# Kernel optimization log

Measured on AMD Instinct MI355X. Metric: run time of the kernel, lower is better.

Reference implementation:

```python
import jax, jax.numpy as jnp
import numpy as np

NUM_GROUPS = 32
EPS = 1e-6


def setup_inputs() -> dict:
    key = jax.random.key(0)
    ks = jax.random.split(key, 10)
    B, C, L = 8, 512, 4096
    s = 1.0 / np.sqrt(C)
    x = jax.random.normal(ks[0], (B, C, L), dtype=jnp.float32)
    gn_w = jnp.ones((C,), jnp.float32)
    gn_b = jnp.zeros((C,), jnp.float32)
    wq = jax.random.normal(ks[1], (C, C), jnp.float32) * s
    bq = jax.random.normal(ks[2], (C,), jnp.float32) * 0.01
    wk = jax.random.normal(ks[3], (C, C), jnp.float32) * s
    bk = jax.random.normal(ks[4], (C,), jnp.float32) * 0.01
    wv = jax.random.normal(ks[5], (C, C), jnp.float32) * s
    bv = jax.random.normal(ks[6], (C,), jnp.float32) * 0.01
    wo = jax.random.normal(ks[7], (C, C), jnp.float32) * s
    bo = jax.random.normal(ks[8], (C,), jnp.float32) * 0.01
    return {"x": x, "gn_w": gn_w, "gn_b": gn_b, "wq": wq, "bq": bq,
            "wk": wk, "bk": bk, "wv": wv, "bv": bv, "wo": wo, "bo": bo}


def _group_norm(x, w, b):
    # x: [B, C, L]; normalize over each group's (C/G, L) slice
    B, C, L = x.shape
    g = x.reshape(B, NUM_GROUPS, C // NUM_GROUPS, L)
    mu = jnp.mean(g, axis=(2, 3), keepdims=True)
    var = jnp.var(g, axis=(2, 3), keepdims=True)
    g = (g - mu) * jax.lax.rsqrt(var + EPS)
    return g.reshape(B, C, L) * w[None, :, None] + b[None, :, None]


def _conv1x1(h, w, b):
    # pointwise conv: [B,C,L] x [Cout,Cin] -> [B,Cout,L]
    return jnp.einsum('oc,bcl->bol', w, h) + b[None, :, None]


def reference(x, gn_w, gn_b, wq, bq, wk, bk, wv, bv, wo, bo):
    h = _group_norm(x, gn_w, gn_b)
    q = _conv1x1(h, wq, bq)
    k = _conv1x1(h, wk, bk)
    v = _conv1x1(h, wv, bv)
    B, C, L = q.shape
    scale = jnp.asarray(C, q.dtype) ** -0.5
    # w_[b,i,j] = sum_c q[b,c,i] k[b,c,j]
    w_ = jnp.einsum('bci,bcj->bij', q, k) * scale
    w_ = jax.nn.softmax(w_, axis=2)
    # h[b,c,i] = sum_j v[b,c,j] w_[b,i,j]
    h = jnp.einsum('bcj,bij->bci', v, w_)
    return x + _conv1x1(h, wo, bo)
```

## Files before the change

kernel.cpp:

```cpp
#include <hip/hip_runtime.h>
#include <hip/hip_bf16.h>
#include <math.h>

#define DI __device__ __forceinline__

typedef unsigned short u16;
typedef unsigned int   u32;
typedef unsigned long long u64;
typedef __attribute__((ext_vector_type(8))) short short8;
typedef __attribute__((ext_vector_type(4))) float f32x4;

constexpr int CB = 512;
constexpr int LL = 4096;
constexpr int NG = 32;

DI float bf2f(u16 u) { u32 v = ((u32)u) << 16; float f; __builtin_memcpy(&f, &v, 4); return f; }
DI u16 f2bf(float f) {
  u32 u; __builtin_memcpy(&u, &f, 4);
  u += 0x7fffu + ((u >> 16) & 1u);
  return (u16)(u >> 16);
}

DI void gload16(const void* g, void* l) {
  __builtin_amdgcn_global_load_lds((const __attribute__((address_space(1))) u32*)g,
                                   (__attribute__((address_space(3))) u32*)l, 16, 0, 0);
}

__global__ __launch_bounds__(256) void conv_w(
    const float* __restrict__ wq, const float* __restrict__ wk,
    const float* __restrict__ wv, const float* __restrict__ wo,
    const float* __restrict__ bq, const float* __restrict__ bk,
    const float* __restrict__ bv,
    u16* __restrict__ wqkv, u16* __restrict__ wob, float* __restrict__ bqkv) {
  if (blockIdx.x < 1024) {
    int i = blockIdx.x * 256 + threadIdx.x;
    wqkv[i]          = f2bf(wq[i]);
    wqkv[262144 + i] = f2bf(wk[i]);
    wqkv[524288 + i] = f2bf(wv[i]);
    wob[i]           = f2bf(wo[i]);
  } else {
    for (int j = 0; j < 6; ++j) {
      int idx = j * 256 + threadIdx.x;
      float b = (idx < 512) ? bq[idx] : (idx < 1024) ? bk[idx - 512] : bv[idx - 1024];
      bqkv[idx] = b;
    }
  }
}

__global__ __launch_bounds__(256) void gn_stats(const float* __restrict__ x,
                                                float* __restrict__ stats) {
  const float4* base = (const float4*)(x + (long)blockIdx.x * (16 * LL));
  float s = 0.f, ss = 0.f;
  for (int i = threadIdx.x; i < 16 * LL / 4; i += 256) {
    float4 v = base[i];
    s  += v.x + v.y + v.z + v.w;
    ss += v.x * v.x + v.y * v.y + v.z * v.z + v.w * v.w;
  }
#pragma unroll
  for (int o = 32; o; o >>= 1) { s += __shfl_xor(s, o); ss += __shfl_xor(ss, o); }
  __shared__ float red[8];
  int wv = threadIdx.x >> 6, ln = threadIdx.x & 63;
  if (ln == 0) { red[wv * 2] = s; red[wv * 2 + 1] = ss; }
  __syncthreads();
  if (threadIdx.x == 0) {
    float S = red[0] + red[2] + red[4] + red[6];
    float SS = red[1] + red[3] + red[5] + red[7];
    float mu = S * (1.f / 65536.f);
    float var = SS * (1.f / 65536.f) - mu * mu;
    stats[blockIdx.x * 2]     = mu;
    stats[blockIdx.x * 2 + 1] = rsqrtf(var + 1e-6f);
  }
}

__global__ __launch_bounds__(256) void gn_apply(
    const float* __restrict__ x, const float* __restrict__ gw,
    const float* __restrict__ gb, const float* __restrict__ stats,
    u16* __restrict__ hT) {
  __shared__ u16 t[64][66];
  const int b = blockIdx.z, c0 = blockIdx.y * 64, l0 = blockIdx.x * 64;
  const int ln = threadIdx.x & 63, sub = threadIdx.x >> 6;
  for (int cr = sub; cr < 64; cr += 4) {
    int c = c0 + cr;
    float v  = x[(long)b * CB * LL + (long)c * LL + l0 + ln];
    float mu = stats[(b * NG + (c >> 4)) * 2];
    float rs = stats[(b * NG + (c >> 4)) * 2 + 1];
    t[cr][ln] = f2bf((v - mu) * rs * gw[c] + gb[c]);
  }
  __syncthreads();
  for (int lr = sub; lr < 64; lr += 4)
    hT[(long)b * LL * CB + (long)(l0 + lr) * CB + c0 + ln] = t[ln][lr];
}

template <int Q>
DI void rdA(const u16* LB, int wr, int fr, int fq, short8 af[2][2]) {
#pragma unroll
  for (int m2 = 0; m2 < 2; ++m2)
#pragma unroll
    for (int kk = 0; kk < 2; ++kk) {
      const int R = wr * 128 + (Q * 2 + m2) * 16 + fr;
      af[m2][kk] = *(const short8*)((const char*)LB + R * 128 +
                                    ((kk * 64 + fq * 16) ^ ((R & 7) << 4)));
    }
}
DI void rdB(const u16* LB, int wc, int fr, int fq, short8 bf[4][2]) {
#pragma unroll
  for (int nf = 0; nf < 4; ++nf)
#pragma unroll
    for (int kk = 0; kk < 2; ++kk) {
      const int R = wc * 64 + nf * 16 + fr;
      bf[nf][kk] = *(const short8*)((const char*)LB + R * 128 +
                                    ((kk * 64 + fq * 16) ^ ((R & 7) << 4)));
    }
}
template <int Q>
DI void mmaQ(short8 af[2][2], short8 bf[4][2], f32x4 acc[8][4]) {
#pragma unroll
  for (int kk = 0; kk < 2; ++kk)
#pragma unroll
    for (int m2 = 0; m2 < 2; ++m2)
#pragma unroll
      for (int nf = 0; nf < 4; ++nf)
        acc[Q * 2 + m2][nf] = __builtin_amdgcn_mfma_f32_16x16x32_bf16(
            af[m2][kk], bf[nf][kk], acc[Q * 2 + m2][nf], 0, 0, 0);
}

#define PTAIL(Q)                                             \
  __builtin_amdgcn_s_barrier();                              \
  asm volatile("s_waitcnt lgkmcnt(0)" ::: "memory");         \
  __builtin_amdgcn_sched_barrier(0);                         \
  __builtin_amdgcn_s_setprio(1);                             \
  mmaQ<Q>(af, bf, acc);                                      \
  __builtin_amdgcn_s_setprio(0);                             \
  __builtin_amdgcn_s_barrier();

template <int EPI>
__global__ __launch_bounds__(512, 2) void gemm8p(
    const u16* __restrict__ A, int lda, long asb,
    const u16* __restrict__ Bt, int ldb, long bsb,
    int K, const float* __restrict__ bias, float scale,
    u16* __restrict__ o0, u16* __restrict__ o1, u16* __restrict__ o2,
    long osb, int ldo) {
  __shared__ u16 smem[65536];
  u16* lA0 = smem;
  u16* lA1 = smem + 16384;
  u16* lB0 = smem + 32768;
  u16* lB1 = smem + 49152;

  const int tid = threadIdx.x;
  const int lane = tid & 63, wv = tid >> 6;
  const int wr = wv >> 2, wc = wv & 3;
  const int fr = lane & 15, fq = lane >> 4;
  const int bx = blockIdx.x, by = blockIdx.y, bz = blockIdx.z;

  const u16* Ab = A + (long)bz * asb + (long)(by * 256) * lda;
  const u16* Bb = Bt + (long)bz * bsb + (long)(bx * 256) * ldb;

  auto stage = [&](u16* lbase, const u16* gbase, int ld_, int half, int t) {
#pragma unroll
    for (int p = 0; p < 2; ++p) {
      int i = p * 512 + tid;
      int row = i >> 3, ch = i & 7;
      int src = t * 64 + ((((ch << 4) ^ ((row & 7) << 4))) >> 1);
      gload16(gbase + (long)(half * 128 + row) * ld_ + src,
              lbase + half * 8192 + i * 8);
    }
  };

  f32x4 acc[8][4];
#pragma unroll
  for (int m = 0; m < 8; ++m)
#pragma unroll
    for (int n = 0; n < 4; ++n) acc[m][n] = (f32x4)(0.f);

  stage(lA0, Ab, lda, 0, 0); stage(lA0, Ab, lda, 1, 0);
  stage(lB0, Bb, ldb, 0, 0); stage(lB0, Bb, ldb, 1, 0);
  stage(lB1, Bb, ldb, 0, 1); stage(lB1, Bb, ldb, 1, 1);
  asm volatile("s_waitcnt vmcnt(4)" ::: "memory");
  __builtin_amdgcn_sched_barrier(0);
  __builtin_amdgcn_s_barrier();

  const int nt = K >> 6;
  short8 af[2][2], bf[4][2];
  for (int i = 0; i < nt / 2; ++i) {
    const bool last = (i == nt / 2 - 1);
    const int t1 = 2 * i + 1, t2 = 2 * i + 2, t3 = 2 * i + 3;
    rdB(lB0, wc, fr, fq, bf);
    rdA<0>(lA0, wr, fr, fq, af);
    stage(lA1, Ab, lda, 0, t1);
    PTAIL(0)
    rdA<1>(lA0, wr, fr, fq, af);
    stage(lA1, Ab, lda, 1, t1);
    PTAIL(1)
    rdA<2>(lA0, wr, fr, fq, af);
    if (!last) stage(lB0, Bb, ldb, 0, t2);
    PTAIL(2)
    rdA<3>(lA0, wr, fr, fq, af);
    if (!last) stage(lB0, Bb, ldb, 1, t2);
    if (last) { asm volatile("s_waitcnt vmcnt(0)" ::: "memory"); }
    else      { asm volatile("s_waitcnt vmcnt(4)" ::: "memory"); }
    __builtin_amdgcn_sched_barrier(0);
    PTAIL(3)
    rdB(lB1, wc, fr, fq, bf);
    rdA<0>(lA1, wr, fr, fq, af);
    if (!last) stage(lA0, Ab, lda, 0, t2);
    PTAIL(0)
    rdA<1>(lA1, wr, fr, fq, af);
    if (!last) stage(lA0, Ab, lda, 1, t2);
    PTAIL(1)
    rdA<2>(lA1, wr, fr, fq, af);
    if (!last) stage(lB1, Bb, ldb, 0, t3);
    PTAIL(2)
    rdA<3>(lA1, wr, fr, fq, af);
    if (!last) stage(lB1, Bb, ldb, 1, t3);
    if (!last) {
      asm volatile("s_waitcnt vmcnt(4)" ::: "memory");
      __builtin_amdgcn_sched_barrier(0);
    }
    PTAIL(3)
  }

  if constexpr (EPI == 1) {
#pragma unroll
    for (int mf = 0; mf < 8; ++mf)
#pragma unroll
      for (int nf = 0; nf < 4; ++nf) {
        const int nl = wc * 64 + nf * 16 + fr;
#pragma unroll
        for (int r = 0; r < 4; ++r) {
          const int ml = wr * 128 + mf * 16 + fq * 4 + r;
          smem[ml * 256 + (nl ^ ((ml & 7) << 3))] =
              f2bf(exp2f(acc[mf][nf][r] * scale));
        }
      }
    __syncthreads();
    u16* dst0 = o0 + (long)bz * osb + (long)(by * 256) * ldo + bx * 256;
    for (int i = tid * 8; i < 65536; i += 4096) {
      const int rr = i >> 8, cc = i & 255;
      short8 val = *(const short8*)&smem[rr * 256 + (cc ^ ((rr & 7) << 3))];
      *(short8*)(dst0 + (long)rr * ldo + cc) = val;
    }
  } else {
    const int mat = by >> 1;
    if (mat < 2) {
#pragma unroll
      for (int mf = 0; mf < 8; ++mf)
#pragma unroll
        for (int nf = 0; nf < 4; ++nf) {
          const int nl = wc * 64 + nf * 16 + fr;
#pragma unroll
          for (int r = 0; r < 4; ++r) {
            const int ml = wr * 128 + mf * 16 + fq * 4 + r;
            smem[nl * 256 + (ml ^ ((nl & 7) << 3))] =
                f2bf(acc[mf][nf][r] + bias[by * 256 + ml]);
          }
        }
      __syncthreads();
      u16* dst0 = (mat == 0 ? o0 : o1) + (long)bz * ((long)LL * CB) +
                  (long)(bx * 256) * CB + ((by * 256) & 511);
      for (int i = tid * 8; i < 65536; i += 4096) {
        const int rr = i >> 8, cc = i & 255;
        short8 val = *(const short8*)&smem[rr * 256 + (cc ^ ((rr & 7) << 3))];
        *(short8*)(dst0 + (long)rr * CB + cc) = val;
      }
    } else {
#pragma unroll
      for (int mf = 0; mf < 8; ++mf)
#pragma unroll
        for (int nf = 0; nf < 4; ++nf) {
          const int nl = wc * 64 + nf * 16 + fr;
#pragma unroll
          for (int r = 0; r < 4; ++r) {
            const int ml = wr * 128 + mf * 16 + fq * 4 + r;
            smem[ml * 256 + (nl ^ ((ml & 7) << 3))] =
                f2bf(acc[mf][nf][r] + bias[by * 256 + ml]);
          }
        }
      __syncthreads();
      u16* dst0 = o2 + (long)bz * ((long)CB * LL) +
                  (long)((by * 256) & 511) * LL + bx * 256;
      for (int i = tid * 8; i < 65536; i += 4096) {
        const int rr = i >> 8, cc = i & 255;
        short8 val = *(const short8*)&smem[rr * 256 + (cc ^ ((rr & 7) << 3))];
        *(short8*)(dst0 + (long)rr * LL + cc) = val;
      }
    }
  }
}

template <int BM, int BN, int EPI, bool SWZ, int WR, int WC>
__global__ __launch_bounds__(WR * WC * 64) void gemm_bt(
    const u16* __restrict__ A, int lda, long asb,
    const u16* __restrict__ Bt, int ldb, long bsb,
    int K, const float* __restrict__ bias, float scale,
    u16* __restrict__ o0, u16* __restrict__ o1, u16* __restrict__ o2,
    float* __restrict__ of, const float* __restrict__ xres, long osb, int ldo) {
  constexpr int NT = WR * WC * 64;
  constexpr int FM = BM / WR / 16, FN = BN / WC / 16;
  static_assert((BM * 8) % NT == 0 && (BN * 8) % NT == 0, "staging div");
  __shared__ u16 smem[(BM + BN) * 64];
  u16* lA = smem;
  u16* lB = smem + BM * 64;

  int bx = blockIdx.x, by = blockIdx.y;
  if constexpr (SWZ) {
    const int nwg = gridDim.x * gridDim.y;
    const int id = by * gridDim.x + bx;
    const int id2 = (id & 7) * (nwg >> 3) + (id >> 3);
    bx = id2 % gridDim.x;
    by = id2 / gridDim.x;
  }

  const int tid = threadIdx.x;
  const int lane = tid & 63;
  const int wv = tid >> 6;
  const int wr = wv / WC, wc = wv % WC;
  const int fr = lane & 15, fq = lane >> 4;
  const int bz = blockIdx.z;
  const int bzb  = (EPI == 4) ? (bz >> 1) : bz;
  const int kbeg = (EPI == 4) ? (bz & 1) * K : 0;

  const u16* Ab = A + (long)bzb * asb + (long)(by * BM) * lda;
  const u16* Bb = Bt + (long)bzb * bsb + (long)(bx * BN) * ldb;

  f32x4 acc[FM][FN];
#pragma unroll
  for (int m = 0; m < FM; ++m)
#pragma unroll
    for (int n = 0; n < FN; ++n) acc[m][n] = (f32x4)(0.f);

  for (int k0 = kbeg; k0 < kbeg + K; k0 += 64) {
#pragma unroll
    for (int p = 0; p < BM * 8 / NT; ++p) {
      int t = p * NT + tid;
      int row = t >> 3;
      int cbl = ((t & 7) << 4) ^ ((row & 7) << 4);
      gload16(Ab + (long)row * lda + k0 + (cbl >> 1), &lA[t * 8]);
    }
#pragma unroll
    for (int p = 0; p < BN * 8 / NT; ++p) {
      int t = p * NT + tid;
      int row = t >> 3;
      int cbl = ((t & 7) << 4) ^ ((row & 7) << 4);
      gload16(Bb + (long)row * ldb + k0 + (cbl >> 1), &lB[t * 8]);
    }
    __syncthreads();
#pragma unroll
    for (int ks = 0; ks < 2; ++ks) {
      short8 af[FM], bfr[FN];
#pragma unroll
      for (int m = 0; m < FM; ++m) {
        int row = wr * (BM / WR) + m * 16 + fr;
        int cb = (ks * 64 + fq * 16) ^ ((row & 7) << 4);
        af[m] = *(const short8*)((const char*)lA + row * 128 + cb);
      }
#pragma unroll
      for (int n = 0; n < FN; ++n) {
        int row = wc * (BN / WC) + n * 16 + fr;
        int cb = (ks * 64 + fq * 16) ^ ((row & 7) << 4);
        bfr[n] = *(const short8*)((const char*)lB + row * 128 + cb);
      }
#pragma unroll
      for (int m = 0; m < FM; ++m)
#pragma unroll
        for (int n = 0; n < FN; ++n)
          acc[m][n] = __builtin_amdgcn_mfma_f32_16x16x32_bf16(af[m], bfr[n], acc[m][n], 0, 0, 0);
    }
    __syncthreads();
  }

  const int ml0 = wr * (BM / WR);
  const int nl0 = wc * (BN / WC);

  if constexpr (EPI == 3) {
    const int mg0 = by * BM + ml0;
    const int ng0 = bx * BN + nl0;
#pragma unroll
    for (int m = 0; m < FM; ++m)
#pragma unroll
      for (int n = 0; n < FN; ++n) {
        const int ng = ng0 + n * 16 + fr;
#pragma unroll
        for (int r = 0; r < 4; ++r) {
          const int mg = mg0 + m * 16 + fq * 4 + r;
          const long off = (long)bz * osb + (long)mg * ldo + ng;
          of[off] = acc[m][n][r] + bias[mg] + xres[off];
        }
      }
  } else {
    const float* rls = xres + (long)(bz >> 1) * LL + by * BM;
#pragma unroll
    for (int m = 0; m < FM; ++m)
#pragma unroll
      for (int n = 0; n < FN; ++n) {
        const int nl = nl0 + n * 16 + fr;
#pragma unroll
        for (int r = 0; r < 4; ++r) {
          const int ml = ml0 + m * 16 + fq * 4 + r;
          smem[ml * BN + (nl ^ ((ml & 7) << 3))] = f2bf(acc[m][n][r] * rls[ml]);
        }
      }
    __syncthreads();
    u16* dst0 = ((bz & 1) ? o1 : o0) + (long)(bz >> 1) * ((long)LL * CB) +
                (long)(by * BM) * ldo + bx * BN;
    for (int i = tid * 8; i < BM * BN; i += NT * 8) {
      const int rr = i / BN, cc = i % BN;
      short8 val = *(const short8*)&smem[rr * BN + (cc ^ ((rr & 7) << 3))];
      *(short8*)(dst0 + (long)rr * ldo + cc) = val;
    }
  }
}

__global__ __launch_bounds__(256) void rsum_rows(const u16* __restrict__ S,
                                                 float* __restrict__ rls) {
  const u16* row = S + ((long)blockIdx.y * LL + blockIdx.x) * LL;
  const int tid = threadIdx.x;
  const int wv = tid >> 6, ln = tid & 63;
  short8 a = ((const short8*)row)[tid * 2];
  short8 b = ((const short8*)row)[tid * 2 + 1];
  float s = 0.f;
#pragma unroll
  for (int j = 0; j < 8; ++j) s += bf2f((u16)a[j]) + bf2f((u16)b[j]);
#pragma unroll
  for (int o = 32; o; o >>= 1) s += __shfl_xor(s, o);
  __shared__ float red[4];
  if (ln == 0) red[wv] = s;
  __syncthreads();
  if (tid == 0)
    rls[(long)blockIdx.y * LL + blockIdx.x] =
        1.0f / (red[0] + red[1] + red[2] + red[3]);
}

__global__ __launch_bounds__(256) void reduce_pp(
    const u16* __restrict__ p0, const u16* __restrict__ p1, u16* __restrict__ o) {
  const long base = (long)blockIdx.y * ((long)LL * CB) +
                    (long)(blockIdx.x * 256 + threadIdx.x) * 16;
#pragma unroll
  for (int h = 0; h < 2; ++h) {
    short8 a = *(const short8*)(p0 + base + h * 8);
    short8 b = *(const short8*)(p1 + base + h * 8);
    short8 r;
#pragma unroll
    for (int j = 0; j < 8; ++j)
      r[j] = (short)f2bf(bf2f((u16)a[j]) + bf2f((u16)b[j]));
    *(short8*)(o + base + h * 8) = r;
  }
}

extern "C" void kernel_launch(void* const* d_in, const int* in_sizes, int n_in,
                              void* d_out, int out_size, void* d_ws, size_t ws_size,
                              hipStream_t stream) {
  const float* x   = (const float*)d_in[0];
  const float* gnw = (const float*)d_in[1];
  const float* gnb = (const float*)d_in[2];
  const float* wq  = (const float*)d_in[3];
  const float* bq  = (const float*)d_in[4];
  const float* wk  = (const float*)d_in[5];
  const float* bk  = (const float*)d_in[6];
  const float* wv  = (const float*)d_in[7];
  const float* bv  = (const float*)d_in[8];
  const float* wo  = (const float*)d_in[9];
  const float* bo  = (const float*)d_in[10];
  float* out = (float*)d_out;

  char* ws = (char*)d_ws;
  const long NEL = (long)LL * CB;
  const long SEL = (long)LL * LL;
  float* stats = (float*)ws;
  float* bqkv  = (float*)(ws + 8192);
  u16* wqkv = (u16*)(ws + 16384);
  u16* wob  = (u16*)(ws + 16384 + 1572864);
  float* rlsm = (float*)(ws + (3l << 20));
  u16* hT   = (u16*)(ws + (4l << 20));
  u16* qT   = hT + 8 * NEL;
  u16* kT   = qT + 8 * NEL;
  u16* vN   = kT + 8 * NEL;
  const size_t base = (4ul << 20) + 4ul * 8 * NEL * 2;

  int G;
  u16 *Sbuf, *aT;
  if (ws_size >= base + 2ul * SEL * 2) G = 2;
  else                                 G = 1;
  if (G > 1) { Sbuf = (u16*)(ws + base); aT = hT; }
  else       { Sbuf = hT; aT = qT; }

  conv_w<<<1025, 256, 0, stream>>>(wq, wk, wv, wo, bq, bk, bv, wqkv, wob, bqkv);
  gn_stats<<<256, 256, 0, stream>>>(x, stats);
  gn_apply<<<dim3(64, 8, 8), 256, 0, stream>>>(x, gnw, gnb, stats, hT);

  gemm8p<0><<<dim3(16, 6, 8), 512, 0, stream>>>(
      wqkv, 512, 0, hT, 512, NEL, 512, bqkv, 1.f, qT, kT, vN, 0, 0);

  const float cl = (1.0f / sqrtf(512.0f)) * 1.44269504f;
  for (int g0 = 0; g0 < 8; g0 += G) {
    gemm8p<1><<<dim3(16, 16, G), 512, 0, stream>>>(
        qT + (long)g0 * NEL, 512, NEL, kT + (long)g0 * NEL, 512, NEL, 512,
        nullptr, cl, Sbuf, nullptr, nullptr, SEL, LL);
    rsum_rows<<<dim3(LL, G), 256, 0, stream>>>(Sbuf, rlsm);
    gemm_bt<128, 128, 4, true, 2, 4><<<dim3(4, 32, 2 * G), 512, 0, stream>>>(
        Sbuf, LL, SEL, vN + (long)g0 * NEL, LL, NEL, 2048,
        nullptr, 1.f, qT + (long)g0 * NEL, kT + (long)g0 * NEL, nullptr,
        nullptr, rlsm, 0, CB);
    reduce_pp<<<dim3(512, G), 256, 0, stream>>>(
        qT + (long)g0 * NEL, kT + (long)g0 * NEL, aT + (long)g0 * NEL);
  }

  gemm_bt<128, 128, 3, false, 2, 2><<<dim3(32, 4, 8), 256, 0, stream>>>(
      wob, 512, 0, aT, 512, NEL, 512, bo, 1.f,
      nullptr, nullptr, nullptr, out, x, NEL, LL);

  (void)in_sizes; (void)n_in; (void)out_size; (void)ws_size;
}
```

Measured before the change: 619.0 us.

## Use 256x256 pipelined gemm8p with 4-way split-K for P·V stage

Adds an EPI==2 epilogue to the 256x256 gemm8p kernel so that the attention-weights times V product runs through it with split-K over four chunks of 1024. Each split writes a bf16 partial scaled by the reciprocal row sum into a scratch buffer laid out at stride 2048, and a new reduce4 kernel sums the four partials into qT. The older 128x128 gemm_bt split-2 path is kept as a fallback for G==1. The aim is to reuse the faster larger-tile pipeline for this GEMM. The cost is more partial-sum traffic and an extra bf16 rounding on each partial.

```diff
diff --git a/kernel.cpp b/kernel.cpp
--- a/kernel.cpp
+++ b/kernel.cpp
@@ -13,6 +13,7 @@
 constexpr int CB = 512;
 constexpr int LL = 4096;
 constexpr int NG = 32;
+constexpr long NELC = (long)LL * CB;
 
 DI float bf2f(u16 u) { u32 v = ((u32)u) << 16; float f; __builtin_memcpy(&f, &v, 4); return f; }
 DI u16 f2bf(float f) {
@@ -139,7 +140,7 @@
     const u16* __restrict__ Bt, int ldb, long bsb,
     int K, const float* __restrict__ bias, float scale,
     u16* __restrict__ o0, u16* __restrict__ o1, u16* __restrict__ o2,
-    long osb, int ldo) {
+    const float* __restrict__ rls, long osb, int ldo) {
   __shared__ u16 smem[65536];
   u16* lA0 = smem;
   u16* lA1 = smem + 16384;
@@ -151,9 +152,11 @@
   const int wr = wv >> 2, wc = wv & 3;
   const int fr = lane & 15, fq = lane >> 4;
   const int bx = blockIdx.x, by = blockIdx.y, bz = blockIdx.z;
-
-  const u16* Ab = A + (long)bz * asb + (long)(by * 256) * lda;
-  const u16* Bb = Bt + (long)bz * bsb + (long)(bx * 256) * ldb;
+  const int bzb = (EPI == 2) ? (bz >> 2) : bz;
+  const int tb  = (EPI == 2) ? (bz & 3) * (K >> 6) : 0;
+
+  const u16* Ab = A + (long)bzb * asb + (long)(by * 256) * lda;
+  const u16* Bb = Bt + (long)bzb * bsb + (long)(bx * 256) * ldb;
 
   auto stage = [&](u16* lbase, const u16* gbase, int ld_, int half, int t) {
 #pragma unroll
@@ -172,9 +175,9 @@
 #pragma unroll
     for (int n = 0; n < 4; ++n) acc[m][n] = (f32x4)(0.f);
 
-  stage(lA0, Ab, lda, 0, 0); stage(lA0, Ab, lda, 1, 0);
-  stage(lB0, Bb, ldb, 0, 0); stage(lB0, Bb, ldb, 1, 0);
-  stage(lB1, Bb, ldb, 0, 1); stage(lB1, Bb, ldb, 1, 1);
+  stage(lA0, Ab, lda, 0, tb); stage(lA0, Ab, lda, 1, tb);
+  stage(lB0, Bb, ldb, 0, tb); stage(lB0, Bb, ldb, 1, tb);
+  stage(lB1, Bb, ldb, 0, tb + 1); stage(lB1, Bb, ldb, 1, tb + 1);
   asm volatile("s_waitcnt vmcnt(4)" ::: "memory");
   __builtin_amdgcn_sched_barrier(0);
   __builtin_amdgcn_s_barrier();
@@ -183,7 +186,7 @@
   short8 af[2][2], bf[4][2];
   for (int i = 0; i < nt / 2; ++i) {
     const bool last = (i == nt / 2 - 1);
-    const int t1 = 2 * i + 1, t2 = 2 * i + 2, t3 = 2 * i + 3;
+    const int t1 = tb + 2 * i + 1, t2 = tb + 2 * i + 2, t3 = tb + 2 * i + 3;
     rdB(lB0, wc, fr, fq, bf);
     rdA<0>(lA0, wr, fr, fq, af);
     stage(lA1, Ab, lda, 0, t1);
@@ -239,6 +242,28 @@
       short8 val = *(const short8*)&smem[rr * 256 + (cc ^ ((rr & 7) << 3))];
       *(short8*)(dst0 + (long)rr * ldo + cc) = val;
     }
+  } else if constexpr (EPI == 2) {
+    const float* rl = rls + (long)bzb * LL + by * 256;
+#pragma unroll
+    for (int mf = 0; mf < 8; ++mf)
+#pragma unroll
+      for (int nf = 0; nf < 4; ++nf) {
+        const int nl = wc * 64 + nf * 16 + fr;
+#pragma unroll
+        for (int r = 0; r < 4; ++r) {
+          const int ml = wr * 128 + mf * 16 + fq * 4 + r;
+          smem[ml * 256 + (nl ^ ((ml & 7) << 3))] =
+              f2bf(acc[mf][nf][r] * rl[ml]);
+        }
+      }
+    __syncthreads();
+    u16* dst0 = o0 + (long)bzb * 4 * NELC + (long)(by * 256) * 2048 +
+                (bz & 3) * 512 + bx * 256;
+    for (int i = tid * 8; i < 65536; i += 4096) {
+      const int rr = i >> 8, cc = i & 255;
+      short8 val = *(const short8*)&smem[rr * 256 + (cc ^ ((rr & 7) << 3))];
+      *(short8*)(dst0 + (long)rr * 2048 + cc) = val;
+    }
   } else {
     const int mat = by >> 1;
     if (mat < 2) {
@@ -255,7 +280,7 @@
           }
         }
       __syncthreads();
-      u16* dst0 = (mat == 0 ? o0 : o1) + (long)bz * ((long)LL * CB) +
+      u16* dst0 = (mat == 0 ? o0 : o1) + (long)bz * NELC +
                   (long)(bx * 256) * CB + ((by * 256) & 511);
       for (int i = tid * 8; i < 65536; i += 4096) {
         const int rr = i >> 8, cc = i & 255;
@@ -400,7 +425,7 @@
         }
       }
     __syncthreads();
-    u16* dst0 = ((bz & 1) ? o1 : o0) + (long)(bz >> 1) * ((long)LL * CB) +
+    u16* dst0 = ((bz & 1) ? o1 : o0) + (long)(bz >> 1) * NELC +
                 (long)(by * BM) * ldo + bx * BN;
     for (int i = tid * 8; i < BM * BN; i += NT * 8) {
       const int rr = i / BN, cc = i % BN;
@@ -430,9 +455,29 @@
         1.0f / (red[0] + red[1] + red[2] + red[3]);
 }
 
+__global__ __launch_bounds__(256) void reduce4(
+    const u16* __restrict__ P, u16* __restrict__ o) {
+  const int b = blockIdx.y;
+  const long idx = (long)blockIdx.x * 256 + threadIdx.x;
+  const int i = (int)(idx >> 6);
+  const int c0 = ((int)idx & 63) * 8;
+  const u16* Pb = P + (long)b * 4 * NELC + (long)i * 2048;
+  float s[8] = {0.f, 0.f, 0.f, 0.f, 0.f, 0.f, 0.f, 0.f};
+#pragma unroll
+  for (int c4 = 0; c4 < 4; ++c4) {
+    short8 v = *(const short8*)(Pb + c4 * 512 + c0);
+#pragma unroll
+    for (int j = 0; j < 8; ++j) s[j] += bf2f((u16)v[j]);
+  }
+  short8 r;
+#pragma unroll
+  for (int j = 0; j < 8; ++j) r[j] = (short)f2bf(s[j]);
+  *(short8*)(o + (long)b * NELC + (long)i * 512 + c0) = r;
+}
+
 __global__ __launch_bounds__(256) void reduce_pp(
     const u16* __restrict__ p0, const u16* __restrict__ p1, u16* __restrict__ o) {
-  const long base = (long)blockIdx.y * ((long)LL * CB) +
+  const long base = (long)blockIdx.y * NELC +
                     (long)(blockIdx.x * 256 + threadIdx.x) * 16;
 #pragma unroll
   for (int h = 0; h < 2; ++h) {
@@ -463,7 +508,7 @@
   float* out = (float*)d_out;
 
   char* ws = (char*)d_ws;
-  const long NEL = (long)LL * CB;
+  const long NEL = NELC;
   const long SEL = (long)LL * LL;
   float* stats = (float*)ws;
   float* bqkv  = (float*)(ws + 8192);
@@ -476,36 +521,39 @@
   u16* vN   = kT + 8 * NEL;
   const size_t base = (4ul << 20) + 4ul * 8 * NEL * 2;
 
-  int G;
-  u16 *Sbuf, *aT;
-  if (ws_size >= base + 2ul * SEL * 2) G = 2;
-  else                                 G = 1;
-  if (G > 1) { Sbuf = (u16*)(ws + base); aT = hT; }
-  else       { Sbuf = hT; aT = qT; }
+  const int G = (ws_size >= base + 2ul * SEL * 2) ? 2 : 1;
+  u16* Sbuf = (G == 2) ? (u16*)(ws + base) : hT;
 
   conv_w<<<1025, 256, 0, stream>>>(wq, wk, wv, wo, bq, bk, bv, wqkv, wob, bqkv);
   gn_stats<<<256, 256, 0, stream>>>(x, stats);
   gn_apply<<<dim3(64, 8, 8), 256, 0, stream>>>(x, gnw, gnb, stats, hT);
 
   gemm8p<0><<<dim3(16, 6, 8), 512, 0, stream>>>(
-      wqkv, 512, 0, hT, 512, NEL, 512, bqkv, 1.f, qT, kT, vN, 0, 0);
+      wqkv, 512, 0, hT, 512, NEL, 512, bqkv, 1.f, qT, kT, vN, nullptr, 0, 0);
 
   const float cl = (1.0f / sqrtf(512.0f)) * 1.44269504f;
   for (int g0 = 0; g0 < 8; g0 += G) {
     gemm8p<1><<<dim3(16, 16, G), 512, 0, stream>>>(
         qT + (long)g0 * NEL, 512, NEL, kT + (long)g0 * NEL, 512, NEL, 512,
-        nullptr, cl, Sbuf, nullptr, nullptr, SEL, LL);
+        nullptr, cl, Sbuf, nullptr, nullptr, nullptr, SEL, LL);
     rsum_rows<<<dim3(LL, G), 256, 0, stream>>>(Sbuf, rlsm);
-    gemm_bt<128, 128, 4, true, 2, 4><<<dim3(4, 32, 2 * G), 512, 0, stream>>>(
-        Sbuf, LL, SEL, vN + (long)g0 * NEL, LL, NEL, 2048,
-        nullptr, 1.f, qT + (long)g0 * NEL, kT + (long)g0 * NEL, nullptr,
-        nullptr, rlsm, 0, CB);
-    reduce_pp<<<dim3(512, G), 256, 0, stream>>>(
-        qT + (long)g0 * NEL, kT + (long)g0 * NEL, aT + (long)g0 * NEL);
+    if (G == 2) {
+      gemm8p<2><<<dim3(2, 16, 8), 512, 0, stream>>>(
+          Sbuf, LL, SEL, vN + (long)g0 * NEL, LL, NEL, 1024,
+          nullptr, 1.f, hT, nullptr, nullptr, rlsm, 0, 0);
+      reduce4<<<dim3(1024, 2), 256, 0, stream>>>(hT, qT + (long)g0 * NEL);
+    } else {
+      gemm_bt<128, 128, 4, true, 2, 4><<<dim3(4, 32, 2), 512, 0, stream>>>(
+          Sbuf, LL, SEL, vN + (long)g0 * NEL, LL, NEL, 2048,
+          nullptr, 1.f, qT + (long)g0 * NEL, kT + (long)g0 * NEL, nullptr,
+          nullptr, rlsm, 0, CB);
+      reduce_pp<<<dim3(512, 1), 256, 0, stream>>>(
+          qT + (long)g0 * NEL, kT + (long)g0 * NEL, qT + (long)g0 * NEL);
+    }
   }
 
   gemm_bt<128, 128, 3, false, 2, 2><<<dim3(32, 4, 8), 256, 0, stream>>>(
-      wob, 512, 0, aT, 512, NEL, 512, bo, 1.f,
+      wob, 512, 0, qT, 512, NEL, 512, bo, 1.f,
       nullptr, nullptr, nullptr, out, x, NEL, LL);
 
   (void)in_sizes; (void)n_in; (void)out_size; (void)ws_size;
```

Measured after the change: 597.5 us. -3.5%, faster.
